# Kernel optimization log

Hardware: AMD Instinct MI355X
Metric: run time of the kernel (lower is better)

Reference implementation:

```python
import jax, jax.numpy as jnp
import numpy as np

N_NODES = 50000
N_EDGES = 800000
N_GRAPHS = 64
D = 64            # input_dim == hidden_dim == output_dim
N_GIN = 4         # num_layers - 1 GINConv layers
N_PRED = 5        # num_layers prediction heads
BN_EPS = 1e-5


def setup_inputs() -> dict:
    key = jax.random.key(0)
    ks = jax.random.split(key, 12)
    x = jax.random.normal(ks[0], (N_NODES, D), dtype=jnp.float32)
    edge_index = jax.random.randint(ks[1], (2, N_EDGES), 0, N_NODES, dtype=jnp.int32)
    # contiguous graph ids covering all N_GRAPHS segments (PyG batch vector)
    batch = ((jnp.arange(N_NODES) * N_GRAPHS) // N_NODES).astype(jnp.int32)
    s = 1.0 / np.sqrt(D)
    mlp_W1 = jax.random.uniform(ks[2], (N_GIN, D, D), jnp.float32, -s, s)
    mlp_b1 = jax.random.uniform(ks[3], (N_GIN, D), jnp.float32, -s, s)
    mlp_W2 = jax.random.uniform(ks[4], (N_GIN, D, D), jnp.float32, -s, s)
    mlp_b2 = jax.random.uniform(ks[5], (N_GIN, D), jnp.float32, -s, s)
    bn_gamma = jnp.ones((N_GIN, D), jnp.float32)
    bn_beta = jnp.zeros((N_GIN, D), jnp.float32)
    prelu_alpha = jnp.float32(0.25)  # nn.PReLU default, shared across layers
    pred_W = jax.random.uniform(ks[6], (N_PRED, D, D), jnp.float32, -s, s)
    pred_b = jax.random.uniform(ks[7], (N_PRED, D), jnp.float32, -s, s)
    return {
        "x": x, "edge_index": edge_index, "batch": batch,
        "mlp_W1": mlp_W1, "mlp_b1": mlp_b1, "mlp_W2": mlp_W2, "mlp_b2": mlp_b2,
        "bn_gamma": bn_gamma, "bn_beta": bn_beta, "prelu_alpha": prelu_alpha,
        "pred_W": pred_W, "pred_b": pred_b,
    }


def reference(x, edge_index, batch, mlp_W1, mlp_b1, mlp_W2, mlp_b2,
              bn_gamma, bn_beta, prelu_alpha, pred_W, pred_b):
    src, dst = edge_index[0], edge_index[1]
    h = x
    hidden_rep = [h]
    for l in range(N_GIN):
        # GINConv, eps = 0 (learn_eps=False): (1+eps)*x_i + sum_{j->i} x_j
        agg = jax.ops.segment_sum(h[src], dst, num_segments=N_NODES)
        z = h + agg
        # 2-layer MLP: Linear -> ReLU -> Linear
        z = jax.nn.relu(z @ mlp_W1[l] + mlp_b1[l])
        z = z @ mlp_W2[l] + mlp_b2[l]
        # BatchNorm1d over nodes (training-mode batch stats)
        mean = z.mean(axis=0)
        var = z.var(axis=0)
        z = (z - mean) * jax.lax.rsqrt(var + BN_EPS) * bn_gamma[l] + bn_beta[l]
        # shared single-parameter PReLU
        h = jnp.where(z > 0, z, prelu_alpha * z)
        hidden_rep.append(h)
    # per-layer max graph pooling + linear head (dropout_prob=0 -> identity)
    reps = []
    for l, hr in enumerate(hidden_rep):
        pooled = jax.ops.segment_max(hr, batch, num_segments=N_GRAPHS)
        reps.append(pooled @ pred_W[l] + pred_b[l])
    # torch.stack(dim=-1) -> (B, D, L), 'cat' aggregation flattens to (B, D*L)
    return jnp.stack(reps, axis=-1).reshape(N_GRAPHS, -1)
```

## Files before the change

kernel.cpp:

```cpp
#include <hip/hip_runtime.h>
#include <hip/hip_bf16.h>

#define N_NODES 50000
#define N_EDGES 800000
#define N_GRAPHS 64
#define DIM 64
#define N_GIN 4
#define N_PRED 5
#define BN_EPS 1e-5f
#define MM_BLOCKS 782
#define NB 625
#define BUCKET_SZ 80
#define POOL_CH 16

typedef short bf16x8 __attribute__((ext_vector_type(8)));
typedef float f32x4 __attribute__((ext_vector_type(4)));

__device__ __forceinline__ float b2f(__hip_bfloat16 v) { return __bfloat162float(v); }

__device__ __forceinline__ float loadv(const void* p, size_t i, int isb) {
    return isb ? b2f(((const __hip_bfloat16*)p)[i]) : ((const float*)p)[i];
}

__device__ __forceinline__ unsigned short f2bu(float f) {
    __hip_bfloat16 h = __float2bfloat16(f);
    return *(unsigned short*)&h;
}
__device__ __forceinline__ float bu2f(unsigned short u) {
    __hip_bfloat16 h = *(__hip_bfloat16*)&u;
    return b2f(h);
}

__device__ __forceinline__ unsigned int enc_f(float f) {
    unsigned int b = __float_as_uint(f);
    return (b & 0x80000000u) ? ~b : (b | 0x80000000u);
}
__device__ __forceinline__ float dec_f(unsigned int u) {
    unsigned int b = (u & 0x80000000u) ? (u ^ 0x80000000u) : ~u;
    return __uint_as_float(b);
}

__device__ __forceinline__ unsigned int gstart(unsigned int g) {
    return (g * (unsigned int)N_NODES + (N_GRAPHS - 1)) >> 6;
}

__global__ void detect_dtype(const unsigned int* __restrict__ xw, int* __restrict__ flag) {
    __shared__ int cnt[256];
    int t = threadIdx.x;
    int c = 0;
    for (int i = t; i < 1024; i += 256) {
        unsigned int e = (xw[i] >> 7) & 0xFFu;
        if (e >= 0x70u && e <= 0x85u) c++;
    }
    cnt[t] = c;
    __syncthreads();
    for (int s = 128; s > 0; s >>= 1) {
        if (t < s) cnt[t] += cnt[t + s];
        __syncthreads();
    }
    if (t == 0) *flag = (cnt[0] >= 512) ? 1 : 0;
}

__global__ void zero_u32(unsigned int* __restrict__ p, int n) {
    int i = blockIdx.x * blockDim.x + threadIdx.x;
    if (i < n) p[i] = 0u;
}

__global__ __launch_bounds__(256) void convert_pool_bg(
    const void* __restrict__ x, unsigned short* __restrict__ H,
    unsigned int* __restrict__ poolEnc, const int* __restrict__ dflag) {
    __shared__ float shmx[4][64];
    int isb = *dflag;
    unsigned int g = blockIdx.x / POOL_CH, p = blockIdx.x % POOL_CH;
    unsigned int s = gstart(g), e = gstart(g + 1), len = e - s;
    unsigned int rs = s + (len * p) / POOL_CH, re = s + (len * (p + 1)) / POOL_CH;
    int r = threadIdx.x >> 6, c = threadIdx.x & 63;
    float mx = -3.0e38f;
    for (unsigned int row = rs + r; row < re; row += 4) {
        float v = loadv(x, (size_t)row * DIM + c, isb);
        H[(size_t)row * DIM + c] = f2bu(v);
        mx = fmaxf(mx, v);
    }
    shmx[r][c] = mx;
    __syncthreads();
    if (threadIdx.x < 64) {
        float m = fmaxf(fmaxf(shmx[0][c], shmx[1][c]), fmaxf(shmx[2][c], shmx[3][c]));
        atomicMax(&poolEnc[g * DIM + c], enc_f(m));
    }
}


__global__ __launch_bounds__(256) void bucket_hist(const int* __restrict__ dst,
                                                   unsigned int* __restrict__ bucketCnt) {
    __shared__ unsigned int h[NB];
    for (int i = threadIdx.x; i < NB; i += 256) h[i] = 0u;
    __syncthreads();
    for (int e = blockIdx.x * 256 + threadIdx.x; e < N_EDGES; e += gridDim.x * 256)
        atomicAdd(&h[(unsigned int)dst[e] / BUCKET_SZ], 1u);
    __syncthreads();
    for (int i = threadIdx.x; i < NB; i += 256) {
        unsigned int v = h[i];
        if (v) atomicAdd(&bucketCnt[i], v);
    }
}

__global__ void scan_buckets(const unsigned int* __restrict__ bucketCnt,
                             unsigned int* __restrict__ bucketBase,
                             unsigned int* __restrict__ bucketCur) {
    __shared__ unsigned int s[256];
    int t = threadIdx.x;
    int i0 = t * 3;
    unsigned int v0 = (i0 < NB) ? bucketCnt[i0] : 0u;
    unsigned int v1 = (i0 + 1 < NB) ? bucketCnt[i0 + 1] : 0u;
    unsigned int v2 = (i0 + 2 < NB) ? bucketCnt[i0 + 2] : 0u;
    unsigned int tsum = v0 + v1 + v2;
    s[t] = tsum;
    __syncthreads();
    for (int off = 1; off < 256; off <<= 1) {
        unsigned int u = (t >= off) ? s[t - off] : 0u;
        __syncthreads();
        s[t] += u;
        __syncthreads();
    }
    unsigned int ex = s[t] - tsum;
    if (i0 < NB)     { bucketBase[i0] = ex;          bucketCur[i0] = ex; }
    if (i0 + 1 < NB) { bucketBase[i0 + 1] = ex + v0; bucketCur[i0 + 1] = ex + v0; }
    if (i0 + 2 < NB) { bucketBase[i0 + 2] = ex + v0 + v1; bucketCur[i0 + 2] = ex + v0 + v1; }
}

__global__ __launch_bounds__(256) void bucket_scatter(
    const int* __restrict__ src, const int* __restrict__ dst,
    unsigned int* __restrict__ bucketCur, uint2* __restrict__ ebuf) {
    __shared__ unsigned int h[NB];
    __shared__ unsigned int base[NB];
    for (int i = threadIdx.x; i < NB; i += 256) h[i] = 0u;
    __syncthreads();
    for (int e = blockIdx.x * 256 + threadIdx.x; e < N_EDGES; e += gridDim.x * 256)
        atomicAdd(&h[(unsigned int)dst[e] / BUCKET_SZ], 1u);
    __syncthreads();
    for (int i = threadIdx.x; i < NB; i += 256) {
        unsigned int v = h[i];
        base[i] = v ? atomicAdd(&bucketCur[i], v) : 0u;
        h[i] = 0u;
    }
    __syncthreads();
    for (int e = blockIdx.x * 256 + threadIdx.x; e < N_EDGES; e += gridDim.x * 256) {
        unsigned int d = (unsigned int)dst[e];
        unsigned int b = d / BUCKET_SZ;
        unsigned int off = atomicAdd(&h[b], 1u);
        ebuf[base[b] + off] = make_uint2((unsigned int)src[e], d);
    }
}

__global__ __launch_bounds__(256) void bucket_csr(
    const uint2* __restrict__ ebuf, const unsigned int* __restrict__ bucketBase,
    const unsigned int* __restrict__ bucketCnt, unsigned int* __restrict__ deg,
    unsigned int* __restrict__ cur, unsigned int* __restrict__ srclist) {
    __shared__ unsigned int ldeg[BUCKET_SZ], lcur[BUCKET_SZ], lscan[BUCKET_SZ];
    int b = blockIdx.x;
    unsigned int ebase = bucketBase[b];
    unsigned int ecnt = bucketCnt[b];
    unsigned int nbase = (unsigned int)b * BUCKET_SZ;
    int t = threadIdx.x;
    if (t < BUCKET_SZ) ldeg[t] = 0u;
    __syncthreads();
    for (unsigned int i = t; i < ecnt; i += 256)
        atomicAdd(&ldeg[ebuf[ebase + i].y - nbase], 1u);
    __syncthreads();
    if (t < BUCKET_SZ) lscan[t] = ldeg[t];
    __syncthreads();
    for (int off = 1; off < BUCKET_SZ; off <<= 1) {
        unsigned int u = 0u;
        if (t < BUCKET_SZ && t >= off) u = lscan[t - off];
        __syncthreads();
        if (t < BUCKET_SZ) lscan[t] += u;
        __syncthreads();
    }
    if (t < BUCKET_SZ) {
        lcur[t] = lscan[t] - ldeg[t];
        deg[nbase + t] = ldeg[t];
        cur[nbase + t] = ebase + lscan[t];
    }
    __syncthreads();
    for (unsigned int i = t; i < ecnt; i += 256) {
        uint2 e = ebuf[ebase + i];
        unsigned int off = atomicAdd(&lcur[e.y - nbase], 1u);
        srclist[ebase + off] = e.x;
    }
}


__global__ void pack_w(const void* __restrict__ W1, const void* __restrict__ W2,
                       unsigned short* __restrict__ P, const int* __restrict__ dflag) {
    int isb = *dflag;
    int mi = blockIdx.x;
    const void* src = (mi < 4) ? W1 : W2;
    size_t off = (size_t)(mi & 3) * 4096;
    for (int it = 0; it < 16; it++) {
        int idx = it * 256 + threadIdx.x;
        int j = idx & 7, l = (idx >> 3) & 63, s = (idx >> 9) & 1, t = idx >> 10;
        int k = s * 32 + (l >> 4) * 8 + j;
        int n = t * 16 + (l & 15);
        P[(size_t)mi * 4096 + idx] = f2bu(loadv(src, off + (size_t)k * 64 + n, isb));
    }
}

__global__ __launch_bounds__(256) void gather_agg8(
    const unsigned short* __restrict__ H, unsigned short* __restrict__ Xb,
    const unsigned int* __restrict__ cur, const unsigned int* __restrict__ deg,
    const unsigned int* __restrict__ srclist) {
    int lane = threadIdx.x & 63;
    int w = threadIdx.x >> 6;
    int node = blockIdx.x * 4 + w;
    int g8 = lane >> 3;
    int t8 = lane & 7;
    unsigned int cnt = deg[node];
    unsigned int start = cur[node] - cnt;
    const unsigned int* sl = srclist + start;
    float a[8] = {0.f, 0.f, 0.f, 0.f, 0.f, 0.f, 0.f, 0.f};
    if (g8 == 0) {
        bf16x8 sv = *(const bf16x8*)&H[(size_t)node * DIM + t8 * 8];
#pragma unroll
        for (int k = 0; k < 8; k++) a[k] = bu2f((unsigned short)sv[k]);
    }
    for (unsigned int j = g8; j < cnt; j += 8) {
        unsigned int s = sl[j];
        bf16x8 v = *(const bf16x8*)&H[(size_t)s * DIM + t8 * 8];
#pragma unroll
        for (int k = 0; k < 8; k++) a[k] += bu2f((unsigned short)v[k]);
    }
#pragma unroll
    for (int k = 0; k < 8; k++) {
        a[k] += __shfl_xor(a[k], 8);
        a[k] += __shfl_xor(a[k], 16);
        a[k] += __shfl_xor(a[k], 32);
    }
    if (g8 == 0) {
        bf16x8 o;
#pragma unroll
        for (int k = 0; k < 8; k++) o[k] = (short)f2bu(a[k]);
        *(bf16x8*)&Xb[(size_t)node * DIM + t8 * 8] = o;
    }
}

__global__ __launch_bounds__(256) void fused_mm(
    const unsigned short* __restrict__ Xb,
    const unsigned short* __restrict__ P1, const unsigned short* __restrict__ P2,
    const void* __restrict__ b1, size_t b1Off, const void* __restrict__ b2, size_t b2Off,
    unsigned short* __restrict__ Zb, float* __restrict__ part,
    const int* __restrict__ dflag) {
    __shared__ __align__(16) short T2[4][16][72];
    __shared__ float S1[4][64], S2[4][64];
    int isb = *dflag;
    int tid = threadIdx.x;
    int lane = tid & 63;
    int w = tid >> 6;
    int r0 = blockIdx.x * 64 + w * 16;
    bool valid = (r0 < N_NODES);
    int m = lane & 15, q = lane >> 4;
    int row = valid ? (r0 + m) : m;

    const bf16x8* Xv = (const bf16x8*)Xb;
    bf16x8 a0 = Xv[(size_t)row * 8 + q];
    bf16x8 a1 = Xv[(size_t)row * 8 + 4 + q];
    const bf16x8* P1v = (const bf16x8*)P1;
    const bf16x8* P2v = (const bf16x8*)P2;
    bf16x8 w1[8], w2[8];
#pragma unroll
    for (int i = 0; i < 8; i++) {
        w1[i] = P1v[(size_t)i * 64 + lane];
        w2[i] = P2v[(size_t)i * 64 + lane];
    }

    f32x4 acc[4] = {{0.f, 0.f, 0.f, 0.f}, {0.f, 0.f, 0.f, 0.f},
                    {0.f, 0.f, 0.f, 0.f}, {0.f, 0.f, 0.f, 0.f}};
#pragma unroll
    for (int t = 0; t < 4; t++) {
        acc[t] = __builtin_amdgcn_mfma_f32_16x16x32_bf16(a0, w1[t * 2 + 0], acc[t], 0, 0, 0);
        acc[t] = __builtin_amdgcn_mfma_f32_16x16x32_bf16(a1, w1[t * 2 + 1], acc[t], 0, 0, 0);
    }
#pragma unroll
    for (int t = 0; t < 4; t++) {
        int col = t * 16 + m;
        float bv = loadv(b1, b1Off + col, isb);
#pragma unroll
        for (int reg = 0; reg < 4; reg++) {
            float v = acc[t][reg] + bv;
            v = v > 0.0f ? v : 0.0f;
            T2[w][q * 4 + reg][col] = (short)f2bu(v);
        }
    }

    bf16x8 c0 = *(const bf16x8*)&T2[w][m][q * 8];
    bf16x8 c1 = *(const bf16x8*)&T2[w][m][32 + q * 8];
    f32x4 acc2[4] = {{0.f, 0.f, 0.f, 0.f}, {0.f, 0.f, 0.f, 0.f},
                     {0.f, 0.f, 0.f, 0.f}, {0.f, 0.f, 0.f, 0.f}};
#pragma unroll
    for (int t = 0; t < 4; t++) {
        acc2[t] = __builtin_amdgcn_mfma_f32_16x16x32_bf16(c0, w2[t * 2 + 0], acc2[t], 0, 0, 0);
        acc2[t] = __builtin_amdgcn_mfma_f32_16x16x32_bf16(c1, w2[t * 2 + 1], acc2[t], 0, 0, 0);
    }

    float s1[4], s2[4];
#pragma unroll
    for (int t = 0; t < 4; t++) {
        float a = 0.0f, b = 0.0f;
        if (valid) {
            int col = t * 16 + m;
            float bv = loadv(b2, b2Off + col, isb);
            int rbase = r0 + q * 4;
#pragma unroll
            for (int reg = 0; reg < 4; reg++) {
                float z = acc2[t][reg] + bv;
                Zb[(size_t)(rbase + reg) * DIM + col] = f2bu(z);
                a += z;
                b += z * z;
            }
        }
        s1[t] = a;
        s2[t] = b;
    }
#pragma unroll
    for (int t = 0; t < 4; t++) {
        s1[t] += __shfl_xor(s1[t], 16);
        s1[t] += __shfl_xor(s1[t], 32);
        s2[t] += __shfl_xor(s2[t], 16);
        s2[t] += __shfl_xor(s2[t], 32);
    }
    if (q == 0) {
#pragma unroll
        for (int t = 0; t < 4; t++) {
            S1[w][t * 16 + m] = s1[t];
            S2[w][t * 16 + m] = s2[t];
        }
    }
    __syncthreads();
    if (tid < 128) {
        int c = tid & 63;
        float v = (tid < 64) ? (S1[0][c] + S1[1][c] + S1[2][c] + S1[3][c])
                             : (S2[0][c] + S2[1][c] + S2[2][c] + S2[3][c]);
        part[(size_t)blockIdx.x * 128 + tid] = v;
    }
}

__global__ void stats_finalize(const float* __restrict__ part,
                               const void* __restrict__ gamma, const void* __restrict__ beta,
                               size_t gOff, float* __restrict__ scsh,
                               const int* __restrict__ dflag) {
    __shared__ double sh1[256], sh2[256];
    int c = blockIdx.x;
    int t = threadIdx.x;
    double a1 = 0.0, a2 = 0.0;
    for (int b = t; b < MM_BLOCKS; b += 256) {
        a1 += (double)part[(size_t)b * 128 + c];
        a2 += (double)part[(size_t)b * 128 + 64 + c];
    }
    sh1[t] = a1;
    sh2[t] = a2;
    __syncthreads();
    for (int s = 128; s > 0; s >>= 1) {
        if (t < s) { sh1[t] += sh1[t + s]; sh2[t] += sh2[t + s]; }
        __syncthreads();
    }
    if (t == 0) {
        int isb = *dflag;
        double mean = sh1[0] * (1.0 / N_NODES);
        double var = sh2[0] * (1.0 / N_NODES) - mean * mean;
        float inv = rsqrtf(fmaxf((float)var, 0.0f) + BN_EPS);
        float g = loadv(gamma, gOff + c, isb);
        float bb = loadv(beta, gOff + c, isb);
        scsh[c] = g * inv;
        scsh[64 + c] = bb - (float)mean * g * inv;
    }
}

__global__ __launch_bounds__(256) void bn_prelu_pool_bg(
    const unsigned short* __restrict__ Zb, unsigned short* __restrict__ H,
    const float* __restrict__ scsh, const void* __restrict__ alpha_p,
    unsigned int* __restrict__ poolEnc, const int* __restrict__ dflag) {
    __shared__ float shmx[4][64];
    int isb = *dflag;
    float alpha = loadv(alpha_p, 0, isb);
    unsigned int g = blockIdx.x / POOL_CH, p = blockIdx.x % POOL_CH;
    unsigned int s = gstart(g), e = gstart(g + 1), len = e - s;
    unsigned int rs = s + (len * p) / POOL_CH, re = s + (len * (p + 1)) / POOL_CH;
    int r = threadIdx.x >> 6, c = threadIdx.x & 63;
    float sc = scsh[c], sh = scsh[64 + c];
    float mx = -3.0e38f;
    for (unsigned int row = rs + r; row < re; row += 4) {
        float v = bu2f(Zb[(size_t)row * DIM + c]) * sc + sh;
        v = v > 0.0f ? v : alpha * v;
        H[(size_t)row * DIM + c] = f2bu(v);
        mx = fmaxf(mx, v);
    }
    shmx[r][c] = mx;
    __syncthreads();
    if (threadIdx.x < 64) {
        float m = fmaxf(fmaxf(shmx[0][c], shmx[1][c]), fmaxf(shmx[2][c], shmx[3][c]));
        atomicMax(&poolEnc[g * DIM + c], enc_f(m));
    }
}


__global__ void convert_pool_f(const void* __restrict__ x, float* __restrict__ A,
                               const int* __restrict__ batch,
                               unsigned int* __restrict__ poolEnc,
                               const int* __restrict__ dflag) {
    int isb = *dflag;
    int idx = blockIdx.x * blockDim.x + threadIdx.x;
    if (idx >= N_NODES * DIM) return;
    int i = idx >> 6, c = idx & 63;
    float v = loadv(x, idx, isb);
    A[idx] = v;
    atomicMax(&poolEnc[batch[i] * DIM + c], enc_f(v));
}

__global__ void copy_f4(const float4* __restrict__ A, float4* __restrict__ B, int n4) {
    int i = blockIdx.x * blockDim.x + threadIdx.x;
    if (i < n4) B[i] = A[i];
}

__global__ void edge_scatter(const int* __restrict__ src, const int* __restrict__ dst,
                             const float* __restrict__ A, float* __restrict__ B) {
    int idx = blockIdx.x * blockDim.x + threadIdx.x;
    if (idx >= N_EDGES * 16) return;
    int e = idx >> 4, q = idx & 15;
    int s = src[e], d = dst[e];
    float4 v = ((const float4*)(A + (size_t)s * DIM))[q];
    float* bp = B + (size_t)d * DIM + (q << 2);
    atomicAdd(bp + 0, v.x);
    atomicAdd(bp + 1, v.y);
    atomicAdd(bp + 2, v.z);
    atomicAdd(bp + 3, v.w);
}

template <bool RELU, bool STATS>
__global__ void mm64(const float* __restrict__ X, const void* __restrict__ W, size_t wOff,
                     const void* __restrict__ bias, size_t bOff, float* __restrict__ Y,
                     double* __restrict__ stats, const int* __restrict__ dflag) {
    int isb = *dflag;
    __shared__ float Ws[64][64];
    __shared__ float Xs[4][64];
    __shared__ float Sv[4][64];
    __shared__ float bsh[64];
    int tid = threadIdx.x;
    for (int i = tid; i < 4096; i += 256) Ws[i >> 6][i & 63] = loadv(W, wOff + i, isb);
    if (tid < 64) bsh[tid] = loadv(bias, bOff + tid, isb);
    int r = tid >> 6, d = tid & 63;
    int row = blockIdx.x * 4 + r;
    Xs[r][d] = X[(size_t)row * DIM + d];
    __syncthreads();
    float acc = bsh[d];
#pragma unroll
    for (int k = 0; k < 64; k++) acc += Xs[r][k] * Ws[k][d];
    if (RELU) acc = acc > 0.0f ? acc : 0.0f;
    Y[(size_t)row * DIM + d] = acc;
    if (STATS) {
        Sv[r][d] = acc;
        __syncthreads();
        if (tid < 64) {
            float s = 0.0f, s2 = 0.0f;
#pragma unroll
            for (int rr = 0; rr < 4; rr++) {
                float v = Sv[rr][tid];
                s += v;
                s2 += v * v;
            }
            atomicAdd(&stats[tid], (double)s);
            atomicAdd(&stats[64 + tid], (double)s2);
        }
    }
}

__global__ void bn_prelu_pool_f(const float* __restrict__ Z, float* __restrict__ H,
                                const double* __restrict__ stats,
                                const void* __restrict__ gamma, const void* __restrict__ beta,
                                size_t gOff, const void* __restrict__ alpha_p,
                                const int* __restrict__ batch,
                                unsigned int* __restrict__ poolEnc,
                                const int* __restrict__ dflag) {
    int isb = *dflag;
    int idx = blockIdx.x * blockDim.x + threadIdx.x;
    if (idx >= N_NODES * DIM) return;
    int i = idx >> 6, c = idx & 63;
    double mn = stats[c] * (1.0 / N_NODES);
    double var = stats[64 + c] * (1.0 / N_NODES) - mn * mn;
    float inv = rsqrtf(fmaxf((float)var, 0.0f) + BN_EPS);
    float z = Z[idx];
    float v = (z - (float)mn) * inv * loadv(gamma, gOff + c, isb) + loadv(beta, gOff + c, isb);
    float alpha = loadv(alpha_p, 0, isb);
    v = v > 0.0f ? v : alpha * v;
    H[idx] = v;
    atomicMax(&poolEnc[batch[i] * DIM + c], enc_f(v));
}

__global__ void pred_head(const unsigned int* __restrict__ poolEnc,
                          const void* __restrict__ predW, const void* __restrict__ predB,
                          void* __restrict__ out, const int* __restrict__ dflag) {
    int isb = *dflag;
    int l = blockIdx.x / N_GRAPHS;
    int g = blockIdx.x % N_GRAPHS;
    int d = threadIdx.x;
    __shared__ float ps[64];
    ps[d] = dec_f(poolEnc[(size_t)l * N_GRAPHS * DIM + g * DIM + d]);
    __syncthreads();
    float acc = loadv(predB, (size_t)l * DIM + d, isb);
    size_t wbase = (size_t)l * DIM * DIM;
#pragma unroll
    for (int k = 0; k < 64; k++) acc += ps[k] * loadv(predW, wbase + k * DIM + d, isb);
    int o = g * (DIM * N_PRED) + d * N_PRED + l;
    if (isb) ((__hip_bfloat16*)out)[o] = __float2bfloat16(acc);
    else ((float*)out)[o] = acc;
}

extern "C" void kernel_launch(void* const* d_in, const int* in_sizes, int n_in,
                              void* d_out, int out_size, void* d_ws, size_t ws_size,
                              hipStream_t stream) {
    const void* x     = d_in[0];
    const int*  edge  = (const int*)d_in[1];
    const int*  batch = (const int*)d_in[2];
    const void* W1    = d_in[3];
    const void* b1    = d_in[4];
    const void* W2    = d_in[5];
    const void* b2    = d_in[6];
    const void* gamma = d_in[7];
    const void* beta  = d_in[8];
    const void* alpha = d_in[9];
    const void* pW    = d_in[10];
    const void* pB    = d_in[11];

    float* A = (float*)d_ws;
    float* B = A + (size_t)N_NODES * DIM;
    double* statsF = (double*)(B + (size_t)N_NODES * DIM);
    unsigned int* poolEnc   = (unsigned int*)(statsF + 128);
    unsigned int* bucketCnt = poolEnc + N_PRED * N_GRAPHS * DIM;
    int* dflag = (int*)(bucketCnt + NB);
    unsigned int* deg        = (unsigned int*)(dflag + 1);
    unsigned int* cur        = deg + N_NODES;
    unsigned int* bucketBase = cur + N_NODES;
    unsigned int* bucketCur  = bucketBase + NB;
    unsigned int* srclist    = bucketCur + NB;
    unsigned short* Wpack = (unsigned short*)(srclist + N_EDGES);
    float* part = (float*)(Wpack + 8 * 4096);
    float* scsh = part + (size_t)MM_BLOCKS * 128;
    uint2* ebuf = (uint2*)B;

    size_t needFull = (size_t)((char*)(scsh + 128) - (char*)d_ws);
    bool useMFMA = ws_size >= needFull;

    const int* esrc = edge;
    const int* edst = edge + N_EDGES;
    const int ND = N_NODES * DIM;

    unsigned short* Hb = (unsigned short*)A;
    unsigned short* Xb = Hb + (size_t)N_NODES * DIM;
    unsigned short* Zb = (unsigned short*)B;

    detect_dtype<<<1, 256, 0, stream>>>((const unsigned int*)x, dflag);
    zero_u32<<<(N_PRED * N_GRAPHS * DIM + NB + 255) / 256, 256, 0, stream>>>(
        poolEnc, N_PRED * N_GRAPHS * DIM + NB);

    if (useMFMA) {
        bucket_hist<<<200, 256, 0, stream>>>(edst, bucketCnt);
        scan_buckets<<<1, 256, 0, stream>>>(bucketCnt, bucketBase, bucketCur);
        bucket_scatter<<<200, 256, 0, stream>>>(esrc, edst, bucketCur, ebuf);
        bucket_csr<<<NB, 256, 0, stream>>>(ebuf, bucketBase, bucketCnt, deg, cur, srclist);

        pack_w<<<8, 256, 0, stream>>>(W1, W2, Wpack, dflag);
        convert_pool_bg<<<N_GRAPHS * POOL_CH, 256, 0, stream>>>(x, Hb, poolEnc, dflag);
        for (int l = 0; l < N_GIN; l++) {
            size_t bOff = (size_t)l * DIM;
            gather_agg8<<<N_NODES / 4, 256, 0, stream>>>(Hb, Xb, cur, deg, srclist);
            fused_mm<<<MM_BLOCKS, 256, 0, stream>>>(
                Xb, Wpack + (size_t)l * 4096, Wpack + (size_t)(4 + l) * 4096,
                b1, bOff, b2, bOff, Zb, part, dflag);
            stats_finalize<<<64, 256, 0, stream>>>(part, gamma, beta, bOff, scsh, dflag);
            bn_prelu_pool_bg<<<N_GRAPHS * POOL_CH, 256, 0, stream>>>(
                Zb, Hb, scsh, alpha, poolEnc + (size_t)(l + 1) * N_GRAPHS * DIM, dflag);
        }
    } else {
        convert_pool_f<<<ND / 256, 256, 0, stream>>>(x, A, batch, poolEnc, dflag);
        for (int l = 0; l < N_GIN; l++) {
            size_t wOff = (size_t)l * DIM * DIM;
            size_t bOff = (size_t)l * DIM;
            copy_f4<<<(ND / 4 + 255) / 256, 256, 0, stream>>>((const float4*)A, (float4*)B,
                                                              ND / 4);
            edge_scatter<<<(N_EDGES * 16) / 256, 256, 0, stream>>>(esrc, edst, A, B);
            mm64<true, false><<<N_NODES / 4, 256, 0, stream>>>(B, W1, wOff, b1, bOff, A, nullptr,
                                                               dflag);
            zero_u32<<<1, 256, 0, stream>>>((unsigned int*)statsF, 256);
            mm64<false, true><<<N_NODES / 4, 256, 0, stream>>>(A, W2, wOff, b2, bOff, B, statsF,
                                                               dflag);
            bn_prelu_pool_f<<<ND / 256, 256, 0, stream>>>(
                B, A, statsF, gamma, beta, bOff, alpha, batch,
                poolEnc + (size_t)(l + 1) * N_GRAPHS * DIM, dflag);
        }
    }
    pred_head<<<N_PRED * N_GRAPHS, DIM, 0, stream>>>(poolEnc, pW, pB, d_out, dflag);
}
```

Baseline: 324.2 us.

## Fold BN+PReLU into next gather and pool via per-graph z min/max

Removes the separate bn_prelu_pool kernel. The gather now applies the previous layer's batch-norm affine and PReLU on the fly to the raw Z values, so H is never materialized. Max pooling is recovered from per-graph min and max of Z, tracked with LDS atomics inside the matmul kernel. The monotonic affine followed by PReLU means max(h) is one of the two transformed extremes. This also merges the dtype detection and zero-init launches into one kernel and skips the Z write on the last layer. In exchange, the gather recomputes the affine per edge read (about 16x per node), and the matmul epilogue gains two shared atomics per element.

```diff
diff --git a/kernel.cpp b/kernel.cpp
--- a/kernel.cpp
+++ b/kernel.cpp
@@ -43,22 +43,31 @@
 __device__ __forceinline__ unsigned int gstart(unsigned int g) {
     return (g * (unsigned int)N_NODES + (N_GRAPHS - 1)) >> 6;
 }
-
-__global__ void detect_dtype(const unsigned int* __restrict__ xw, int* __restrict__ flag) {
-    __shared__ int cnt[256];
-    int t = threadIdx.x;
-    int c = 0;
-    for (int i = t; i < 1024; i += 256) {
-        unsigned int e = (xw[i] >> 7) & 0xFFu;
-        if (e >= 0x70u && e <= 0x85u) c++;
-    }
-    cnt[t] = c;
-    __syncthreads();
-    for (int s = 128; s > 0; s >>= 1) {
-        if (t < s) cnt[t] += cnt[t + s];
+__device__ __forceinline__ unsigned int graph_of(unsigned int row) {
+    return (row * (unsigned int)N_GRAPHS) / (unsigned int)N_NODES;
+}
+
+__global__ void init_all(unsigned int* __restrict__ base, int nZero, int nTotal,
+                         const unsigned int* __restrict__ xw, int* __restrict__ flag) {
+    int idx = blockIdx.x * blockDim.x + threadIdx.x;
+    if (idx < nZero) base[idx] = 0u;
+    else if (idx < nTotal) base[idx] = 0xFFFFFFFFu;
+    if (blockIdx.x == 0) {
+        __shared__ int cnt[256];
+        int t = threadIdx.x;
+        int c = 0;
+        for (int i = t; i < 1024; i += 256) {
+            unsigned int e = (xw[i] >> 7) & 0xFFu;
+            if (e >= 0x70u && e <= 0x85u) c++;
+        }
+        cnt[t] = c;
         __syncthreads();
-    }
-    if (t == 0) *flag = (cnt[0] >= 512) ? 1 : 0;
+        for (int s = 128; s > 0; s >>= 1) {
+            if (t < s) cnt[t] += cnt[t + s];
+            __syncthreads();
+        }
+        if (t == 0) *flag = (cnt[0] >= 512) ? 1 : 0;
+    }
 }
 
 __global__ void zero_u32(unsigned int* __restrict__ p, int n) {
@@ -205,29 +214,49 @@
     }
 }
 
-__global__ __launch_bounds__(256) void gather_agg8(
-    const unsigned short* __restrict__ H, unsigned short* __restrict__ Xb,
+__global__ __launch_bounds__(256) void gather_affine(
+    const unsigned short* __restrict__ Zsrc, unsigned short* __restrict__ Xb,
     const unsigned int* __restrict__ cur, const unsigned int* __restrict__ deg,
-    const unsigned int* __restrict__ srclist) {
+    const unsigned int* __restrict__ srclist, const float* __restrict__ scsh,
+    const void* __restrict__ alpha_p, int ident, const int* __restrict__ dflag) {
     int lane = threadIdx.x & 63;
     int w = threadIdx.x >> 6;
     int node = blockIdx.x * 4 + w;
     int g8 = lane >> 3;
     int t8 = lane & 7;
+    float sc[8], sh[8], alpha;
+    if (ident) {
+#pragma unroll
+        for (int k = 0; k < 8; k++) { sc[k] = 1.0f; sh[k] = 0.0f; }
+        alpha = 1.0f;
+    } else {
+#pragma unroll
+        for (int k = 0; k < 8; k++) {
+            sc[k] = scsh[t8 * 8 + k];
+            sh[k] = scsh[64 + t8 * 8 + k];
+        }
+        alpha = loadv(alpha_p, 0, *dflag);
+    }
     unsigned int cnt = deg[node];
     unsigned int start = cur[node] - cnt;
     const unsigned int* sl = srclist + start;
     float a[8] = {0.f, 0.f, 0.f, 0.f, 0.f, 0.f, 0.f, 0.f};
     if (g8 == 0) {
-        bf16x8 sv = *(const bf16x8*)&H[(size_t)node * DIM + t8 * 8];
-#pragma unroll
-        for (int k = 0; k < 8; k++) a[k] = bu2f((unsigned short)sv[k]);
+        bf16x8 sv = *(const bf16x8*)&Zsrc[(size_t)node * DIM + t8 * 8];
+#pragma unroll
+        for (int k = 0; k < 8; k++) {
+            float v = bu2f((unsigned short)sv[k]) * sc[k] + sh[k];
+            a[k] = v > 0.0f ? v : alpha * v;
+        }
     }
     for (unsigned int j = g8; j < cnt; j += 8) {
         unsigned int s = sl[j];
-        bf16x8 v = *(const bf16x8*)&H[(size_t)s * DIM + t8 * 8];
-#pragma unroll
-        for (int k = 0; k < 8; k++) a[k] += bu2f((unsigned short)v[k]);
+        bf16x8 v = *(const bf16x8*)&Zsrc[(size_t)s * DIM + t8 * 8];
+#pragma unroll
+        for (int k = 0; k < 8; k++) {
+            float h = bu2f((unsigned short)v[k]) * sc[k] + sh[k];
+            a[k] += h > 0.0f ? h : alpha * h;
+        }
     }
 #pragma unroll
     for (int k = 0; k < 8; k++) {
@@ -243,22 +272,34 @@
     }
 }
 
+template <bool WRITEZ>
 __global__ __launch_bounds__(256) void fused_mm(
     const unsigned short* __restrict__ Xb,
     const unsigned short* __restrict__ P1, const unsigned short* __restrict__ P2,
     const void* __restrict__ b1, size_t b1Off, const void* __restrict__ b2, size_t b2Off,
     unsigned short* __restrict__ Zb, float* __restrict__ part,
+    unsigned int* __restrict__ zmaxE, unsigned int* __restrict__ zminE,
     const int* __restrict__ dflag) {
     __shared__ __align__(16) short T2[4][16][72];
     __shared__ float S1[4][64], S2[4][64];
+    __shared__ unsigned int zmxL[2][64], zmnL[2][64];
     int isb = *dflag;
     int tid = threadIdx.x;
     int lane = tid & 63;
     int w = tid >> 6;
+    if (tid < 128) {
+        zmxL[tid >> 6][tid & 63] = 0u;
+        zmnL[tid >> 6][tid & 63] = 0xFFFFFFFFu;
+    }
+    __syncthreads();
     int r0 = blockIdx.x * 64 + w * 16;
     bool valid = (r0 < N_NODES);
     int m = lane & 15, q = lane >> 4;
     int row = valid ? (r0 + m) : m;
+    int r0blk = blockIdx.x * 64;
+    unsigned int gLo = graph_of((unsigned int)r0blk);
+    int lastRow = r0blk + 63 > N_NODES - 1 ? N_NODES - 1 : r0blk + 63;
+    unsigned int gHi = graph_of((unsigned int)lastRow);
 
     const bf16x8* Xv = (const bf16x8*)Xb;
     bf16x8 a0 = Xv[(size_t)row * 8 + q];
@@ -312,7 +353,11 @@
 #pragma unroll
             for (int reg = 0; reg < 4; reg++) {
                 float z = acc2[t][reg] + bv;
-                Zb[(size_t)(rbase + reg) * DIM + col] = f2bu(z);
+                if (WRITEZ) Zb[(size_t)(rbase + reg) * DIM + col] = f2bu(z);
+                unsigned int e = enc_f(z);
+                unsigned int gi = graph_of((unsigned int)(rbase + reg)) - gLo;
+                atomicMax(&zmxL[gi][col], e);
+                atomicMin(&zmnL[gi][col], e);
                 a += z;
                 b += z * z;
             }
@@ -340,6 +385,11 @@
         float v = (tid < 64) ? (S1[0][c] + S1[1][c] + S1[2][c] + S1[3][c])
                              : (S2[0][c] + S2[1][c] + S2[2][c] + S2[3][c]);
         part[(size_t)blockIdx.x * 128 + tid] = v;
+        int gi = tid >> 6;
+        if (gLo + gi <= gHi) {
+            atomicMax(&zmaxE[(gLo + gi) * 64 + c], zmxL[gi][c]);
+            atomicMin(&zminE[(gLo + gi) * 64 + c], zmnL[gi][c]);
+        }
     }
 }
 
@@ -371,33 +421,6 @@
         float bb = loadv(beta, gOff + c, isb);
         scsh[c] = g * inv;
         scsh[64 + c] = bb - (float)mean * g * inv;
-    }
-}
-
-__global__ __launch_bounds__(256) void bn_prelu_pool_bg(
-    const unsigned short* __restrict__ Zb, unsigned short* __restrict__ H,
-    const float* __restrict__ scsh, const void* __restrict__ alpha_p,
-    unsigned int* __restrict__ poolEnc, const int* __restrict__ dflag) {
-    __shared__ float shmx[4][64];
-    int isb = *dflag;
-    float alpha = loadv(alpha_p, 0, isb);
-    unsigned int g = blockIdx.x / POOL_CH, p = blockIdx.x % POOL_CH;
-    unsigned int s = gstart(g), e = gstart(g + 1), len = e - s;
-    unsigned int rs = s + (len * p) / POOL_CH, re = s + (len * (p + 1)) / POOL_CH;
-    int r = threadIdx.x >> 6, c = threadIdx.x & 63;
-    float sc = scsh[c], sh = scsh[64 + c];
-    float mx = -3.0e38f;
-    for (unsigned int row = rs + r; row < re; row += 4) {
-        float v = bu2f(Zb[(size_t)row * DIM + c]) * sc + sh;
-        v = v > 0.0f ? v : alpha * v;
-        H[(size_t)row * DIM + c] = f2bu(v);
-        mx = fmaxf(mx, v);
-    }
-    shmx[r][c] = mx;
-    __syncthreads();
-    if (threadIdx.x < 64) {
-        float m = fmaxf(fmaxf(shmx[0][c], shmx[1][c]), fmaxf(shmx[2][c], shmx[3][c]));
-        atomicMax(&poolEnc[g * DIM + c], enc_f(m));
     }
 }
 
@@ -495,14 +518,33 @@
 }
 
 __global__ void pred_head(const unsigned int* __restrict__ poolEnc,
+                          const unsigned int* __restrict__ zmaxE,
+                          const unsigned int* __restrict__ zminE,
+                          const float* __restrict__ scshAll,
+                          const void* __restrict__ alpha_p,
                           const void* __restrict__ predW, const void* __restrict__ predB,
-                          void* __restrict__ out, const int* __restrict__ dflag) {
+                          void* __restrict__ out, const int* __restrict__ dflag,
+                          int useZmm) {
     int isb = *dflag;
     int l = blockIdx.x / N_GRAPHS;
     int g = blockIdx.x % N_GRAPHS;
     int d = threadIdx.x;
     __shared__ float ps[64];
-    ps[d] = dec_f(poolEnc[(size_t)l * N_GRAPHS * DIM + g * DIM + d]);
+    float pv;
+    if (!useZmm || l == 0) {
+        pv = dec_f(poolEnc[(size_t)l * N_GRAPHS * DIM + g * DIM + d]);
+    } else {
+        int s = l - 1;
+        float sc = scshAll[s * 128 + d];
+        float sh = scshAll[s * 128 + 64 + d];
+        float alpha = loadv(alpha_p, 0, isb);
+        float t1 = sc * dec_f(zmaxE[(size_t)s * 4096 + g * 64 + d]) + sh;
+        float t2 = sc * dec_f(zminE[(size_t)s * 4096 + g * 64 + d]) + sh;
+        float h1 = t1 > 0.0f ? t1 : alpha * t1;
+        float h2 = t2 > 0.0f ? t2 : alpha * t2;
+        pv = fmaxf(h1, h2);
+    }
+    ps[d] = pv;
     __syncthreads();
     float acc = loadv(predB, (size_t)l * DIM + d, isb);
     size_t wbase = (size_t)l * DIM * DIM;
@@ -531,21 +573,23 @@
 
     float* A = (float*)d_ws;
     float* B = A + (size_t)N_NODES * DIM;
-    double* statsF = (double*)(B + (size_t)N_NODES * DIM);
-    unsigned int* poolEnc   = (unsigned int*)(statsF + 128);
+    unsigned int* poolEnc   = (unsigned int*)(B + (size_t)N_NODES * DIM);
     unsigned int* bucketCnt = poolEnc + N_PRED * N_GRAPHS * DIM;
-    int* dflag = (int*)(bucketCnt + NB);
+    unsigned int* zmaxE     = bucketCnt + NB;
+    unsigned int* zminE     = zmaxE + 4 * 4096;
+    int* dflag = (int*)(zminE + 4 * 4096);
     unsigned int* deg        = (unsigned int*)(dflag + 1);
     unsigned int* cur        = deg + N_NODES;
     unsigned int* bucketBase = cur + N_NODES;
     unsigned int* bucketCur  = bucketBase + NB;
     unsigned int* srclist    = bucketCur + NB;
     unsigned short* Wpack = (unsigned short*)(srclist + N_EDGES);
-    float* part = (float*)(Wpack + 8 * 4096);
-    float* scsh = part + (size_t)MM_BLOCKS * 128;
+    float* part    = (float*)(Wpack + 8 * 4096);
+    float* scshAll = part + (size_t)MM_BLOCKS * 128;
+    double* statsF = (double*)(scshAll + 512);
     uint2* ebuf = (uint2*)B;
 
-    size_t needFull = (size_t)((char*)(scsh + 128) - (char*)d_ws);
+    size_t needFull = (size_t)((char*)(statsF + 128) - (char*)d_ws);
     bool useMFMA = ws_size >= needFull;
 
     const int* esrc = edge;
@@ -556,9 +600,10 @@
     unsigned short* Xb = Hb + (size_t)N_NODES * DIM;
     unsigned short* Zb = (unsigned short*)B;
 
-    detect_dtype<<<1, 256, 0, stream>>>((const unsigned int*)x, dflag);
-    zero_u32<<<(N_PRED * N_GRAPHS * DIM + NB + 255) / 256, 256, 0, stream>>>(
-        poolEnc, N_PRED * N_GRAPHS * DIM + NB);
+    const int initZeroCnt = N_PRED * N_GRAPHS * DIM + NB + 4 * 4096;
+    const int initTotCnt  = initZeroCnt + 4 * 4096;
+    init_all<<<(initTotCnt + 255) / 256, 256, 0, stream>>>(poolEnc, initZeroCnt, initTotCnt,
+                                                           (const unsigned int*)x, dflag);
 
     if (useMFMA) {
         bucket_hist<<<200, 256, 0, stream>>>(edst, bucketCnt);
@@ -570,14 +615,28 @@
         convert_pool_bg<<<N_GRAPHS * POOL_CH, 256, 0, stream>>>(x, Hb, poolEnc, dflag);
         for (int l = 0; l < N_GIN; l++) {
             size_t bOff = (size_t)l * DIM;
-            gather_agg8<<<N_NODES / 4, 256, 0, stream>>>(Hb, Xb, cur, deg, srclist);
-            fused_mm<<<MM_BLOCKS, 256, 0, stream>>>(
-                Xb, Wpack + (size_t)l * 4096, Wpack + (size_t)(4 + l) * 4096,
-                b1, bOff, b2, bOff, Zb, part, dflag);
-            stats_finalize<<<64, 256, 0, stream>>>(part, gamma, beta, bOff, scsh, dflag);
-            bn_prelu_pool_bg<<<N_GRAPHS * POOL_CH, 256, 0, stream>>>(
-                Zb, Hb, scsh, alpha, poolEnc + (size_t)(l + 1) * N_GRAPHS * DIM, dflag);
-        }
+            if (l == 0)
+                gather_affine<<<N_NODES / 4, 256, 0, stream>>>(
+                    Hb, Xb, cur, deg, srclist, nullptr, alpha, 1, dflag);
+            else
+                gather_affine<<<N_NODES / 4, 256, 0, stream>>>(
+                    Zb, Xb, cur, deg, srclist, scshAll + (size_t)(l - 1) * 128, alpha, 0,
+                    dflag);
+            if (l < 3)
+                fused_mm<true><<<MM_BLOCKS, 256, 0, stream>>>(
+                    Xb, Wpack + (size_t)l * 4096, Wpack + (size_t)(4 + l) * 4096,
+                    b1, bOff, b2, bOff, Zb, part, zmaxE + (size_t)l * 4096,
+                    zminE + (size_t)l * 4096, dflag);
+            else
+                fused_mm<false><<<MM_BLOCKS, 256, 0, stream>>>(
+                    Xb, Wpack + (size_t)l * 4096, Wpack + (size_t)(4 + l) * 4096,
+                    b1, bOff, b2, bOff, Zb, part, zmaxE + (size_t)l * 4096,
+                    zminE + (size_t)l * 4096, dflag);
+            stats_finalize<<<64, 256, 0, stream>>>(part, gamma, beta, bOff,
+                                                   scshAll + (size_t)l * 128, dflag);
+        }
+        pred_head<<<N_PRED * N_GRAPHS, DIM, 0, stream>>>(
+            poolEnc, zmaxE, zminE, scshAll, alpha, pW, pB, d_out, dflag, 1);
     } else {
         convert_pool_f<<<ND / 256, 256, 0, stream>>>(x, A, batch, poolEnc, dflag);
         for (int l = 0; l < N_GIN; l++) {
@@ -595,6 +654,7 @@
                 B, A, statsF, gamma, beta, bOff, alpha, batch,
                 poolEnc + (size_t)(l + 1) * N_GRAPHS * DIM, dflag);
         }
-    }
-    pred_head<<<N_PRED * N_GRAPHS, DIM, 0, stream>>>(poolEnc, pW, pB, d_out, dflag);
-}
+        pred_head<<<N_PRED * N_GRAPHS, DIM, 0, stream>>>(
+            poolEnc, zmaxE, zminE, scshAll, alpha, pW, pB, d_out, dflag, 0);
+    }
+}
```

After: 310.1 us. 4.3% less time.
